# Optimization experiments

Measured on AMD Instinct MI355X. Metric: run time of the kernel, lower is better.

The kernel has to match this reference:

```python
import jax, jax.numpy as jnp
import numpy as np

D_MODEL = 1024
N_HEADS = 16
D_HEAD = D_MODEL // N_HEADS
B, T = 4, 2048


def setup_inputs() -> dict:
    key = jax.random.key(0)
    ks = jax.random.split(key, 7)
    s = 0.02
    q = jax.random.normal(ks[0], (B, T, D_MODEL), dtype=jnp.float32)
    k = jax.random.normal(ks[1], (B, T, D_MODEL), dtype=jnp.float32)
    v = jax.random.normal(ks[2], (B, T, D_MODEL), dtype=jnp.float32)
    # causal mask, True = masked (strict upper triangle)
    mask = jnp.triu(jnp.ones((T, T), dtype=bool), k=1)[None, None, :, :]
    Wq = jax.random.normal(ks[3], (D_MODEL, D_MODEL), dtype=jnp.float32) * s
    Wk = jax.random.normal(ks[4], (D_MODEL, D_MODEL), dtype=jnp.float32) * s
    Wv = jax.random.normal(ks[5], (D_MODEL, D_MODEL), dtype=jnp.float32) * s
    Wo = jax.random.normal(ks[6], (D_MODEL, D_MODEL), dtype=jnp.float32) * s
    return {"q": q, "k": k, "v": v, "mask": mask,
            "Wq": Wq, "Wk": Wk, "Wv": Wv, "Wo": Wo}


def reference(q, k, v, mask, Wq, Wk, Wv, Wo):
    H, Dh = N_HEADS, D_HEAD
    scale = Dh ** -0.5

    def split(t):  # [B,T,D] -> [B,H,T,Dh]
        Bt, Tt, _ = t.shape
        return t.reshape(Bt, Tt, H, Dh).transpose(0, 2, 1, 3)

    # torch Linear (no bias): y = x @ W.T
    Q = split(q @ Wq.T)
    K = split(k @ Wk.T)
    V = split(v @ Wv.T)

    scores = jnp.einsum('bhqd,bhkd->bhqk', Q, K) * scale
    scores = jnp.where(mask, -jnp.inf, scores)
    attn = jax.nn.softmax(scores, axis=-1)
    attn = jnp.nan_to_num(attn)  # fully-masked rows -> 0
    out = jnp.einsum('bhqk,bhkd->bhqd', attn, V)
    out = out.transpose(0, 2, 1, 3).reshape(q.shape[0], q.shape[1], H * Dh)
    return out @ Wo.T
```

## Files before the change

kernel.cpp:

```cpp
#include <hip/hip_runtime.h>
#include <stdint.h>

#define D_MODEL 1024
#define N_HEADS 16
#define D_HEAD 64
#define BATCH 4
#define SEQ 2048
#define MTOT (BATCH * SEQ)

typedef unsigned short u16;
typedef __attribute__((ext_vector_type(8))) short bf16x8;
typedef __attribute__((ext_vector_type(4))) float f32x4;

#define MFMA(a, b, c) __builtin_amdgcn_mfma_f32_16x16x32_bf16((a), (b), (c), 0, 0, 0)
#define LOG2E 1.4426950408889634f
#define SC (0.125f * LOG2E)

static __device__ __forceinline__ u16 f2bf(float f) {
  unsigned u = __builtin_bit_cast(unsigned, f);
  u += 0x7fffu + ((u >> 16) & 1u);
  return (u16)(u >> 16);
}
static __device__ __forceinline__ u16 f2bf_t(float f) {
  return (u16)(__builtin_bit_cast(unsigned, f) >> 16);
}

static __device__ __forceinline__ void gload_lds16(const void* g, void* l) {
  __builtin_amdgcn_global_load_lds(
      (const __attribute__((address_space(1))) void*)g,
      (__attribute__((address_space(3))) void*)l, 16, 0, 0);
}

__global__ __launch_bounds__(256) void cvt3(const float* __restrict__ a,
                                            const float* __restrict__ b,
                                            const float* __restrict__ c,
                                            u16* __restrict__ oa, u16* __restrict__ ob,
                                            u16* __restrict__ oc) {
  const int z = blockIdx.y;
  const float* in = (z == 0) ? a : (z == 1) ? b : c;
  u16* out = (z == 0) ? oa : (z == 1) ? ob : oc;
  int i = blockIdx.x * 256 + threadIdx.x;
  float4 v = ((const float4*)in)[i];
  ushort4 o;
  o.x = f2bf(v.x); o.y = f2bf(v.y); o.z = f2bf(v.z); o.w = f2bf(v.w);
  ((ushort4*)out)[i] = o;
}

__global__ __launch_bounds__(256) void cvt4(const float* __restrict__ a,
                                            const float* __restrict__ b,
                                            const float* __restrict__ c,
                                            const float* __restrict__ d,
                                            u16* __restrict__ oa, u16* __restrict__ ob,
                                            u16* __restrict__ oc, u16* __restrict__ od) {
  const int z = blockIdx.y;
  const float* in = (z == 0) ? a : (z == 1) ? b : (z == 2) ? c : d;
  u16* out = (z == 0) ? oa : (z == 1) ? ob : (z == 2) ? oc : od;
  const float s = (z == 0) ? SC : 1.0f;
  int i = blockIdx.x * 256 + threadIdx.x;
  float4 v = ((const float4*)in)[i];
  ushort4 o;
  o.x = f2bf(v.x * s); o.y = f2bf(v.y * s); o.z = f2bf(v.z * s); o.w = f2bf(v.w * s);
  ((ushort4*)out)[i] = o;
}


__global__ __launch_bounds__(256) void gemm_qkv(const u16* __restrict__ xq,
                                                const u16* __restrict__ xk,
                                                const u16* __restrict__ xv,
                                                const u16* __restrict__ Wqb,
                                                const u16* __restrict__ Wkb,
                                                const u16* __restrict__ Wvb,
                                                u16* __restrict__ Qb, u16* __restrict__ Kb,
                                                u16* __restrict__ Vtg, int zbase) {
  __shared__ u16 As[128 * 64];
  __shared__ u16 Bs[128 * 64];
  const int z = blockIdx.z + zbase;
  const u16* A = (z == 0) ? xq : (z == 1) ? xk : xv;
  const u16* B = (z == 0) ? Wqb : (z == 1) ? Wkb : Wvb;

  const int t = threadIdx.x;
  const int lane = t & 63, wave = t >> 6;
  const int wm = wave & 1, wn = wave >> 1;
  const int lrow = lane & 15, quad = lane >> 4;
  const int m0 = blockIdx.x * 128, n0 = blockIdx.y * 128;
  const int srow = t >> 3;
  const int swcol = (((t & 7) ^ (srow & 7)) << 3);
  const int rsw = lrow & 7;

  f32x4 acc[4][4];
#pragma unroll
  for (int i = 0; i < 4; i++)
#pragma unroll
    for (int j = 0; j < 4; j++) acc[i][j] = (f32x4){0.f, 0.f, 0.f, 0.f};

  for (int k0 = 0; k0 < 1024; k0 += 64) {
#pragma unroll
    for (int r = 0; r < 4; ++r) {
      int rr = r * 32 + srow;
      gload_lds16(A + (size_t)(m0 + rr) * 1024 + k0 + swcol, As + rr * 64 + (t & 7) * 8);
      gload_lds16(B + (size_t)(n0 + rr) * 1024 + k0 + swcol, Bs + rr * 64 + (t & 7) * 8);
    }
    __syncthreads();
#pragma unroll
    for (int ks = 0; ks < 2; ++ks) {
      const int cx = ((ks * 4 + quad) ^ rsw) << 3;
      bf16x8 a[4], b[4];
#pragma unroll
      for (int i = 0; i < 4; i++)
        a[i] = *(const bf16x8*)(As + (wm * 64 + i * 16 + lrow) * 64 + cx);
#pragma unroll
      for (int j = 0; j < 4; j++)
        b[j] = *(const bf16x8*)(Bs + (wn * 64 + j * 16 + lrow) * 64 + cx);
#pragma unroll
      for (int i = 0; i < 4; i++)
#pragma unroll
        for (int j = 0; j < 4; j++) acc[i][j] = MFMA(a[i], b[j], acc[i][j]);
    }
    __syncthreads();
  }
  if (z == 2) {
    const int b = m0 >> 11;
    const int t0 = (m0 & 2047);
#pragma unroll
    for (int i = 0; i < 4; i++) {
      const int trow = t0 + wm * 64 + i * 16 + quad * 4;
#pragma unroll
      for (int j = 0; j < 4; j++) {
        const int n = n0 + wn * 64 + j * 16 + lrow;
        ushort4 pk;
        pk.x = f2bf(acc[i][j][0]); pk.y = f2bf(acc[i][j][1]);
        pk.z = f2bf(acc[i][j][2]); pk.w = f2bf(acc[i][j][3]);
        *(ushort4*)(Vtg + (size_t)b * D_MODEL * SEQ + (size_t)n * SEQ + trow) = pk;
      }
    }
  } else {
    u16* C = z ? Kb : Qb;
#pragma unroll
    for (int i = 0; i < 4; i++) {
      const int mr = m0 + wm * 64 + i * 16 + quad * 4;
#pragma unroll
      for (int j = 0; j < 4; j++) {
        const int n = n0 + wn * 64 + j * 16 + lrow;
#pragma unroll
        for (int r = 0; r < 4; r++) C[(size_t)(mr + r) * 1024 + n] = f2bf(acc[i][j][r]);
      }
    }
  }
}

__global__ __launch_bounds__(256) void gemm_o(const u16* __restrict__ A,
                                              const u16* __restrict__ B,
                                              float* __restrict__ C) {
  __shared__ u16 As[128 * 64];
  __shared__ u16 Bs[128 * 64];
  const int t = threadIdx.x;
  const int lane = t & 63, wave = t >> 6;
  const int wm = wave & 1, wn = wave >> 1;
  const int lrow = lane & 15, quad = lane >> 4;
  const int m0 = blockIdx.x * 128, n0 = blockIdx.y * 128;
  const int srow = t >> 3;
  const int swcol = (((t & 7) ^ (srow & 7)) << 3);
  const int rsw = lrow & 7;

  f32x4 acc[4][4];
#pragma unroll
  for (int i = 0; i < 4; i++)
#pragma unroll
    for (int j = 0; j < 4; j++) acc[i][j] = (f32x4){0.f, 0.f, 0.f, 0.f};

  for (int k0 = 0; k0 < 1024; k0 += 64) {
#pragma unroll
    for (int r = 0; r < 4; ++r) {
      int rr = r * 32 + srow;
      gload_lds16(A + (size_t)(m0 + rr) * 1024 + k0 + swcol, As + rr * 64 + (t & 7) * 8);
      gload_lds16(B + (size_t)(n0 + rr) * 1024 + k0 + swcol, Bs + rr * 64 + (t & 7) * 8);
    }
    __syncthreads();
#pragma unroll
    for (int ks = 0; ks < 2; ++ks) {
      const int cx = ((ks * 4 + quad) ^ rsw) << 3;
      bf16x8 a[4], b[4];
#pragma unroll
      for (int i = 0; i < 4; i++)
        a[i] = *(const bf16x8*)(As + (wm * 64 + i * 16 + lrow) * 64 + cx);
#pragma unroll
      for (int j = 0; j < 4; j++)
        b[j] = *(const bf16x8*)(Bs + (wn * 64 + j * 16 + lrow) * 64 + cx);
#pragma unroll
      for (int i = 0; i < 4; i++)
#pragma unroll
        for (int j = 0; j < 4; j++) acc[i][j] = MFMA(a[i], b[j], acc[i][j]);
    }
    __syncthreads();
  }
#pragma unroll
  for (int i = 0; i < 4; i++) {
    const int mr = m0 + wm * 64 + i * 16 + quad * 4;
#pragma unroll
    for (int j = 0; j < 4; j++) {
      const int n = n0 + wn * 64 + j * 16 + lrow;
#pragma unroll
      for (int r = 0; r < 4; r++) C[(size_t)(mr + r) * 1024 + n] = acc[i][j][r];
    }
  }
}

__global__ __launch_bounds__(256) void attn_causal(const u16* __restrict__ Qb,
                                                   const u16* __restrict__ Kb,
                                                   const u16* __restrict__ Vtg,
                                                   u16* __restrict__ Ob) {
  __shared__ u16 QPs[128 * 64];
  __shared__ u16 Ks[64 * 64];
  __shared__ u16 Vs[64 * 64];

  const int t = threadIdx.x;
  const int lane = t & 63, wave = t >> 6;
  const int lrow = lane & 15, quad = lane >> 4;
  const int wb = wave * 32;
  const int bh = blockIdx.x;
  const int b = bh >> 4, h = bh & 15;
  const int col0 = h * 64;
  const size_t rowbase = (size_t)b * SEQ;
  const size_t vbase = (size_t)b * (size_t)D_MODEL * SEQ;
  const int srow = t >> 3;
  const int swcol = (((t & 7) ^ (srow & 7)) << 3);
  const int pchunk = (t & 7) * 8;
  const int rsw = lrow & 7;

  bf16x8 bOnes;
  {
    const short ov = (lrow == 0) ? (short)0x3F80 : (short)0;
#pragma unroll
    for (int e = 0; e < 8; ++e) bOnes[e] = ov;
  }

  for (int part = 0; part < 2; ++part) {
    const int qt = part ? (15 - (int)blockIdx.y) : (int)blockIdx.y;
    const int qrow0 = qt * 128;

#pragma unroll
    for (int r = 0; r < 4; ++r) {
      int rr = r * 32 + srow;
      gload_lds16(Qb + (rowbase + qrow0 + rr) * D_MODEL + col0 + swcol,
                  QPs + rr * 64 + pchunk);
    }

    bf16x8 bQ[2][2];
    f32x4 oacc[2][4];
    f32x4 lacc[2];
#pragma unroll
    for (int mf = 0; mf < 2; mf++) {
#pragma unroll
      for (int df = 0; df < 4; df++) oacc[mf][df] = (f32x4){0.f, 0.f, 0.f, 0.f};
      lacc[mf] = (f32x4){0.f, 0.f, 0.f, 0.f};
    }

    const int nkt = 2 * qt + 2;
    for (int kt = 0; kt < nkt; ++kt) {
      const int j0 = kt * 64;
      __syncthreads();
#pragma unroll
      for (int r = 0; r < 2; ++r) {
        int rr = r * 32 + srow;
        gload_lds16(Kb + (rowbase + j0 + rr) * D_MODEL + col0 + swcol,
                    Ks + rr * 64 + pchunk);
        gload_lds16(Vtg + vbase + (size_t)(col0 + rr) * SEQ + j0 + swcol,
                    Vs + rr * 64 + pchunk);
      }
      __syncthreads();

      if (kt == 0) {
#pragma unroll
        for (int mf = 0; mf < 2; ++mf)
#pragma unroll
          for (int ks = 0; ks < 2; ++ks)
            bQ[mf][ks] = *(const bf16x8*)(QPs + (wb + mf * 16 + lrow) * 64 +
                                          (((ks * 4 + quad) ^ rsw) << 3));
      }

      const bool diag = (kt >= 2 * qt);
#pragma unroll
      for (int mf = 0; mf < 2; ++mf) {
        f32x4 st[4];
#pragma unroll
        for (int jf = 0; jf < 4; jf++) st[jf] = (f32x4){0.f, 0.f, 0.f, 0.f};
#pragma unroll
        for (int ks = 0; ks < 2; ++ks) {
          const int cx = ((ks * 4 + quad) ^ rsw) << 3;
#pragma unroll
          for (int jf = 0; jf < 4; jf++) {
            bf16x8 aK = *(const bf16x8*)(Ks + (jf * 16 + lrow) * 64 + cx);
            st[jf] = MFMA(aK, bQ[mf][ks], st[jf]);
          }
        }
        const int m = wb + mf * 16 + lrow;
        const int gm = qrow0 + m;
#pragma unroll
        for (int jf = 0; jf < 4; jf++) {
          ushort4 pk;
#pragma unroll
          for (int r = 0; r < 4; r++) {
            float p = __builtin_amdgcn_exp2f(st[jf][r]);
            const int gj = j0 + jf * 16 + quad * 4 + r;
            if (diag && gj > gm) p = 0.f;
            ((u16*)&pk)[r] = f2bf_t(p);
          }
          const int j = jf * 16 + quad * 4;
          *(ushort4*)(QPs + m * 64 + ((((j >> 3) ^ (m & 7)) << 3) | (j & 7))) = pk;
        }
      }

#pragma unroll
      for (int ks = 0; ks < 2; ++ks) {
        const int cx = ((ks * 4 + quad) ^ rsw) << 3;
        bf16x8 aP[2];
#pragma unroll
        for (int mf = 0; mf < 2; ++mf)
          aP[mf] = *(const bf16x8*)(QPs + (wb + mf * 16 + lrow) * 64 + cx);
        lacc[0] = MFMA(aP[0], bOnes, lacc[0]);
        lacc[1] = MFMA(aP[1], bOnes, lacc[1]);
#pragma unroll
        for (int df = 0; df < 4; df++) {
          bf16x8 bV = *(const bf16x8*)(Vs + (df * 16 + lrow) * 64 + cx);
          oacc[0][df] = MFMA(aP[0], bV, oacc[0][df]);
          oacc[1][df] = MFMA(aP[1], bV, oacc[1][df]);
        }
      }
    }
    __syncthreads();

    float linv[2][4];
#pragma unroll
    for (int mf = 0; mf < 2; mf++)
#pragma unroll
      for (int r = 0; r < 4; r++)
        linv[mf][r] = 1.0f / __shfl(lacc[mf][r], lane & 48);

#pragma unroll
    for (int mf = 0; mf < 2; mf++)
#pragma unroll
      for (int r = 0; r < 4; r++) {
        u16* orow = Ob + (rowbase + qrow0 + wb + mf * 16 + quad * 4 + r) * D_MODEL + col0;
#pragma unroll
        for (int df = 0; df < 4; df++)
          orow[df * 16 + lrow] = f2bf(oacc[mf][df][r] * linv[mf][r]);
      }
  }
}

extern "C" void kernel_launch(void* const* d_in, const int* in_sizes, int n_in,
                              void* d_out, int out_size, void* d_ws, size_t ws_size,
                              hipStream_t stream) {
  const float* q  = (const float*)d_in[0];
  const float* k  = (const float*)d_in[1];
  const float* v  = (const float*)d_in[2];
  const float* Wq = (const float*)d_in[4];
  const float* Wk = (const float*)d_in[5];
  const float* Wv = (const float*)d_in[6];
  const float* Wo = (const float*)d_in[7];
  float* out = (float*)d_out;

  char* ws = (char*)d_ws;
  const size_t MB = 1 << 20;
  u16* xq  = (u16*)(ws);
  u16* xk  = (u16*)(ws + 16 * MB);
  u16* xv  = (u16*)(ws + 32 * MB);
  u16* Wqb = (u16*)(ws + 48 * MB);
  u16* Wkb = (u16*)(ws + 50 * MB);
  u16* Wvb = (u16*)(ws + 52 * MB);
  u16* Wob = (u16*)(ws + 54 * MB);
  u16* Qb  = (u16*)(ws + 56 * MB);

  const dim3 cb(256);
  cvt3<<<dim3(MTOT * D_MODEL / 4 / 256, 3), cb, 0, stream>>>(q, k, v, xq, xk, xv);
  cvt4<<<dim3(D_MODEL * D_MODEL / 4 / 256, 4), cb, 0, stream>>>(Wq, Wk, Wv, Wo,
                                                                Wqb, Wkb, Wvb, Wob);

  if (ws_size >= 104 * MB) {
    u16* Kb  = (u16*)(ws + 72 * MB);
    u16* Vtg = (u16*)(ws + 88 * MB);
    gemm_qkv<<<dim3(64, 8, 3), cb, 0, stream>>>(xq, xk, xv, Wqb, Wkb, Wvb,
                                                Qb, Kb, Vtg, 0);
    attn_causal<<<dim3(64, 8), cb, 0, stream>>>(Qb, Kb, Vtg, xq);
    gemm_o<<<dim3(64, 8), cb, 0, stream>>>(xq, Wob, out);
  } else {
    u16* Kb  = (u16*)(ws);
    u16* Vtg = (u16*)(ws + 16 * MB);
    u16* Oatt = (u16*)(ws + 32 * MB);
    gemm_qkv<<<dim3(64, 8, 1), cb, 0, stream>>>(xq, xq, xq, Wqb, Wqb, Wqb,
                                                Qb, Qb, Qb, 0);
    gemm_qkv<<<dim3(64, 8, 1), cb, 0, stream>>>(xk, xk, xk, Wkb, Wkb, Wkb,
                                                Kb, Kb, Kb, 1);
    gemm_qkv<<<dim3(64, 8, 1), cb, 0, stream>>>(xv, xv, xv, Wvb, Wvb, Wvb,
                                                Vtg, Vtg, Vtg, 2);
    attn_causal<<<dim3(64, 8), cb, 0, stream>>>(Qb, Kb, Vtg, Oatt);
    gemm_o<<<dim3(64, 8), cb, 0, stream>>>(Oatt, Wob, out);
  }
}
```

Baseline: 313.8 us.

## Fuse fp32-to-bf16 activation conversion into QKV GEMM and retile output GEMM

Removes the separate cvt3 pass over the fp32 q/k/v activations. The QKV GEMM now loads fp32 rows directly, packs them to bf16 in registers, and writes them into shared memory, which saves a full write and re-read of the bf16 copies. The output projection GEMM is retiled to 128x64 blocks, doubling the grid for better occupancy, and the workspace layout is simplified into a single path. In exchange, A-tile loads are now synchronous register loads instead of direct-to-LDS loads, and twice as many global bytes are read per A tile.

After: 322.9 us. 1.03x slower.

```diff
diff --git a/kernel.cpp b/kernel.cpp
--- a/kernel.cpp
+++ b/kernel.cpp
@@ -1,4 +1,5 @@
 #include <hip/hip_runtime.h>
+#include <hip/hip_bf16.h>
 #include <stdint.h>
 
 #define D_MODEL 1024
@@ -25,25 +26,19 @@
   return (u16)(__builtin_bit_cast(unsigned, f) >> 16);
 }
 
+static __device__ __forceinline__ bf16x8 pack8(float4 a, float4 b) {
+  union { bf16x8 v; __hip_bfloat162 h[4]; } u;
+  u.h[0] = __float22bfloat162_rn(make_float2(a.x, a.y));
+  u.h[1] = __float22bfloat162_rn(make_float2(a.z, a.w));
+  u.h[2] = __float22bfloat162_rn(make_float2(b.x, b.y));
+  u.h[3] = __float22bfloat162_rn(make_float2(b.z, b.w));
+  return u.v;
+}
+
 static __device__ __forceinline__ void gload_lds16(const void* g, void* l) {
   __builtin_amdgcn_global_load_lds(
       (const __attribute__((address_space(1))) void*)g,
       (__attribute__((address_space(3))) void*)l, 16, 0, 0);
-}
-
-__global__ __launch_bounds__(256) void cvt3(const float* __restrict__ a,
-                                            const float* __restrict__ b,
-                                            const float* __restrict__ c,
-                                            u16* __restrict__ oa, u16* __restrict__ ob,
-                                            u16* __restrict__ oc) {
-  const int z = blockIdx.y;
-  const float* in = (z == 0) ? a : (z == 1) ? b : c;
-  u16* out = (z == 0) ? oa : (z == 1) ? ob : oc;
-  int i = blockIdx.x * 256 + threadIdx.x;
-  float4 v = ((const float4*)in)[i];
-  ushort4 o;
-  o.x = f2bf(v.x); o.y = f2bf(v.y); o.z = f2bf(v.z); o.w = f2bf(v.w);
-  ((ushort4*)out)[i] = o;
 }
 
 __global__ __launch_bounds__(256) void cvt4(const float* __restrict__ a,
@@ -64,18 +59,19 @@
 }
 
 
-__global__ __launch_bounds__(256) void gemm_qkv(const u16* __restrict__ xq,
-                                                const u16* __restrict__ xk,
-                                                const u16* __restrict__ xv,
-                                                const u16* __restrict__ Wqb,
-                                                const u16* __restrict__ Wkb,
-                                                const u16* __restrict__ Wvb,
-                                                u16* __restrict__ Qb, u16* __restrict__ Kb,
-                                                u16* __restrict__ Vtg, int zbase) {
+__global__ __launch_bounds__(256, 4) void gemm_qkv(const float* __restrict__ xq,
+                                                   const float* __restrict__ xk,
+                                                   const float* __restrict__ xv,
+                                                   const u16* __restrict__ Wqb,
+                                                   const u16* __restrict__ Wkb,
+                                                   const u16* __restrict__ Wvb,
+                                                   u16* __restrict__ Qb,
+                                                   u16* __restrict__ Kb,
+                                                   u16* __restrict__ Vtg) {
   __shared__ u16 As[128 * 64];
   __shared__ u16 Bs[128 * 64];
-  const int z = blockIdx.z + zbase;
-  const u16* A = (z == 0) ? xq : (z == 1) ? xk : xv;
+  const int z = blockIdx.z;
+  const float* A = (z == 0) ? xq : (z == 1) ? xk : xv;
   const u16* B = (z == 0) ? Wqb : (z == 1) ? Wkb : Wvb;
 
   const int t = threadIdx.x;
@@ -85,6 +81,7 @@
   const int m0 = blockIdx.x * 128, n0 = blockIdx.y * 128;
   const int srow = t >> 3;
   const int swcol = (((t & 7) ^ (srow & 7)) << 3);
+  const int pchunk = (t & 7) * 8;
   const int rsw = lrow & 7;
 
   f32x4 acc[4][4];
@@ -97,8 +94,14 @@
 #pragma unroll
     for (int r = 0; r < 4; ++r) {
       int rr = r * 32 + srow;
-      gload_lds16(A + (size_t)(m0 + rr) * 1024 + k0 + swcol, As + rr * 64 + (t & 7) * 8);
-      gload_lds16(B + (size_t)(n0 + rr) * 1024 + k0 + swcol, Bs + rr * 64 + (t & 7) * 8);
+      gload_lds16(B + (size_t)(n0 + rr) * 1024 + k0 + swcol, Bs + rr * 64 + pchunk);
+    }
+#pragma unroll
+    for (int r = 0; r < 4; ++r) {
+      int rr = r * 32 + srow;
+      const float4* src = (const float4*)(A + (size_t)(m0 + rr) * 1024 + k0 + swcol);
+      float4 fa = src[0], fb = src[1];
+      *(bf16x8*)(As + rr * 64 + pchunk) = pack8(fa, fb);
     }
     __syncthreads();
 #pragma unroll
@@ -152,19 +155,19 @@
                                               const u16* __restrict__ B,
                                               float* __restrict__ C) {
   __shared__ u16 As[128 * 64];
-  __shared__ u16 Bs[128 * 64];
+  __shared__ u16 Bs[64 * 64];
   const int t = threadIdx.x;
   const int lane = t & 63, wave = t >> 6;
-  const int wm = wave & 1, wn = wave >> 1;
   const int lrow = lane & 15, quad = lane >> 4;
-  const int m0 = blockIdx.x * 128, n0 = blockIdx.y * 128;
+  const int m0 = blockIdx.x * 128, n0 = blockIdx.y * 64;
   const int srow = t >> 3;
   const int swcol = (((t & 7) ^ (srow & 7)) << 3);
+  const int pchunk = (t & 7) * 8;
   const int rsw = lrow & 7;
 
-  f32x4 acc[4][4];
-#pragma unroll
-  for (int i = 0; i < 4; i++)
+  f32x4 acc[2][4];
+#pragma unroll
+  for (int i = 0; i < 2; i++)
 #pragma unroll
     for (int j = 0; j < 4; j++) acc[i][j] = (f32x4){0.f, 0.f, 0.f, 0.f};
 
@@ -172,33 +175,37 @@
 #pragma unroll
     for (int r = 0; r < 4; ++r) {
       int rr = r * 32 + srow;
-      gload_lds16(A + (size_t)(m0 + rr) * 1024 + k0 + swcol, As + rr * 64 + (t & 7) * 8);
-      gload_lds16(B + (size_t)(n0 + rr) * 1024 + k0 + swcol, Bs + rr * 64 + (t & 7) * 8);
+      gload_lds16(A + (size_t)(m0 + rr) * 1024 + k0 + swcol, As + rr * 64 + pchunk);
+    }
+#pragma unroll
+    for (int r = 0; r < 2; ++r) {
+      int rr = r * 32 + srow;
+      gload_lds16(B + (size_t)(n0 + rr) * 1024 + k0 + swcol, Bs + rr * 64 + pchunk);
     }
     __syncthreads();
 #pragma unroll
     for (int ks = 0; ks < 2; ++ks) {
       const int cx = ((ks * 4 + quad) ^ rsw) << 3;
-      bf16x8 a[4], b[4];
-#pragma unroll
-      for (int i = 0; i < 4; i++)
-        a[i] = *(const bf16x8*)(As + (wm * 64 + i * 16 + lrow) * 64 + cx);
+      bf16x8 a[2], b[4];
+#pragma unroll
+      for (int i = 0; i < 2; i++)
+        a[i] = *(const bf16x8*)(As + (wave * 32 + i * 16 + lrow) * 64 + cx);
 #pragma unroll
       for (int j = 0; j < 4; j++)
-        b[j] = *(const bf16x8*)(Bs + (wn * 64 + j * 16 + lrow) * 64 + cx);
-#pragma unroll
-      for (int i = 0; i < 4; i++)
+        b[j] = *(const bf16x8*)(Bs + (j * 16 + lrow) * 64 + cx);
+#pragma unroll
+      for (int i = 0; i < 2; i++)
 #pragma unroll
         for (int j = 0; j < 4; j++) acc[i][j] = MFMA(a[i], b[j], acc[i][j]);
     }
     __syncthreads();
   }
 #pragma unroll
-  for (int i = 0; i < 4; i++) {
-    const int mr = m0 + wm * 64 + i * 16 + quad * 4;
+  for (int i = 0; i < 2; i++) {
+    const int mr = m0 + wave * 32 + i * 16 + quad * 4;
 #pragma unroll
     for (int j = 0; j < 4; j++) {
-      const int n = n0 + wn * 64 + j * 16 + lrow;
+      const int n = n0 + j * 16 + lrow;
 #pragma unroll
       for (int r = 0; r < 4; r++) C[(size_t)(mr + r) * 1024 + n] = acc[i][j][r];
     }
@@ -362,38 +369,19 @@
 
   char* ws = (char*)d_ws;
   const size_t MB = 1 << 20;
-  u16* xq  = (u16*)(ws);
-  u16* xk  = (u16*)(ws + 16 * MB);
-  u16* xv  = (u16*)(ws + 32 * MB);
-  u16* Wqb = (u16*)(ws + 48 * MB);
-  u16* Wkb = (u16*)(ws + 50 * MB);
-  u16* Wvb = (u16*)(ws + 52 * MB);
-  u16* Wob = (u16*)(ws + 54 * MB);
-  u16* Qb  = (u16*)(ws + 56 * MB);
+  u16* Oatt = (u16*)(ws);
+  u16* Qb   = (u16*)(ws + 16 * MB);
+  u16* Kb   = (u16*)(ws + 32 * MB);
+  u16* Vtg  = (u16*)(ws + 48 * MB);
+  u16* Wqb  = (u16*)(ws + 64 * MB);
+  u16* Wkb  = (u16*)(ws + 66 * MB);
+  u16* Wvb  = (u16*)(ws + 68 * MB);
+  u16* Wob  = (u16*)(ws + 70 * MB);
 
   const dim3 cb(256);
-  cvt3<<<dim3(MTOT * D_MODEL / 4 / 256, 3), cb, 0, stream>>>(q, k, v, xq, xk, xv);
   cvt4<<<dim3(D_MODEL * D_MODEL / 4 / 256, 4), cb, 0, stream>>>(Wq, Wk, Wv, Wo,
                                                                 Wqb, Wkb, Wvb, Wob);
-
-  if (ws_size >= 104 * MB) {
-    u16* Kb  = (u16*)(ws + 72 * MB);
-    u16* Vtg = (u16*)(ws + 88 * MB);
-    gemm_qkv<<<dim3(64, 8, 3), cb, 0, stream>>>(xq, xk, xv, Wqb, Wkb, Wvb,
-                                                Qb, Kb, Vtg, 0);
-    attn_causal<<<dim3(64, 8), cb, 0, stream>>>(Qb, Kb, Vtg, xq);
-    gemm_o<<<dim3(64, 8), cb, 0, stream>>>(xq, Wob, out);
-  } else {
-    u16* Kb  = (u16*)(ws);
-    u16* Vtg = (u16*)(ws + 16 * MB);
-    u16* Oatt = (u16*)(ws + 32 * MB);
-    gemm_qkv<<<dim3(64, 8, 1), cb, 0, stream>>>(xq, xq, xq, Wqb, Wqb, Wqb,
-                                                Qb, Qb, Qb, 0);
-    gemm_qkv<<<dim3(64, 8, 1), cb, 0, stream>>>(xk, xk, xk, Wkb, Wkb, Wkb,
-                                                Kb, Kb, Kb, 1);
-    gemm_qkv<<<dim3(64, 8, 1), cb, 0, stream>>>(xv, xv, xv, Wvb, Wvb, Wvb,
-                                                Vtg, Vtg, Vtg, 2);
-    attn_causal<<<dim3(64, 8), cb, 0, stream>>>(Qb, Kb, Vtg, Oatt);
-    gemm_o<<<dim3(64, 8), cb, 0, stream>>>(Oatt, Wob, out);
-  }
-}
+  gemm_qkv<<<dim3(64, 8, 3), cb, 0, stream>>>(q, k, v, Wqb, Wkb, Wvb, Qb, Kb, Vtg);
+  attn_causal<<<dim3(64, 8), cb, 0, stream>>>(Qb, Kb, Vtg, Oatt);
+  gemm_o<<<dim3(64, 16), cb, 0, stream>>>(Oatt, Wob, out);
+}
```
